# Performance work log

Measured on AMD Instinct MI355X. Metric: run time of the kernel, lower is better.

Reference implementation:

```python
import jax, jax.numpy as jnp
import numpy as np

D_MODEL = 1024
N_HEAD = 16
SEQ_LEN = 4096


def setup_inputs() -> dict:
    key = jax.random.key(0)
    ks = jax.random.split(key, 5)
    s = 0.02
    return {
        "x": jax.random.normal(ks[0], (SEQ_LEN, D_MODEL), dtype=jnp.float32),
        "w_qkv": jax.random.normal(ks[1], (D_MODEL, 3 * D_MODEL), dtype=jnp.float32) * s,
        "b_qkv": jnp.zeros((3 * D_MODEL,), dtype=jnp.float32),
        "w_o": jax.random.normal(ks[2], (D_MODEL, D_MODEL), dtype=jnp.float32) * s,
        "b_o": jnp.zeros((D_MODEL,), dtype=jnp.float32),
    }


def reference(x, w_qkv, b_qkv, w_o, b_o):
    seq_len, d_model = x.shape
    n_head = N_HEAD
    d_h = d_model // n_head

    qkv = x @ w_qkv + b_qkv                                  # [S, 3D]
    q, k, v = jnp.split(qkv, 3, axis=-1)                     # each [S, D]
    # [S, D] -> [H, S, d_h]
    q = q.reshape(seq_len, n_head, d_h).transpose(1, 0, 2)
    k = k.reshape(seq_len, n_head, d_h).transpose(1, 0, 2)
    v = v.reshape(seq_len, n_head, d_h).transpose(1, 0, 2)

    sim = jnp.einsum("hsd,htd->hst", q, k) / jnp.sqrt(jnp.float32(d_h))  # [H, S, S]
    causal = jnp.tril(jnp.ones((seq_len, seq_len), dtype=bool))[None]    # [1, S, S]
    neg_inf = jnp.finfo(sim.dtype).min
    sim = jnp.where(causal, sim, neg_inf)
    attn = jax.nn.softmax(sim, axis=-1)                                  # [H, S, S]
    out = jnp.einsum("hst,htd->hsd", attn, v)                            # [H, S, d_h]
    out = out.transpose(1, 0, 2).reshape(seq_len, d_model)               # [S, D]
    return out @ w_o + b_o
```

## Files before the change

kernel.cpp:

```cpp
#include <hip/hip_runtime.h>
#include <hip/hip_bf16.h>
#include <stdint.h>

typedef __bf16 bf16_t;
typedef __bf16 bf16x8 __attribute__((ext_vector_type(8)));
typedef float f32x4 __attribute__((ext_vector_type(4)));
typedef float f32x16 __attribute__((ext_vector_type(16)));

#define SEQ_LEN 4096
#define D_MODEL 1024
#define N_HEAD 16



__device__ __forceinline__ void gload_lds16(const void* g, void* lds) {
  __builtin_amdgcn_global_load_lds(
      (__attribute__((address_space(1))) void*)(g),
      (__attribute__((address_space(3))) void*)(lds), 16, 0, 0);
}

__device__ __forceinline__ unsigned short f2bfu(float f) {
  __bf16 h = (__bf16)f;
  return __builtin_bit_cast(unsigned short, h);
}

__device__ __forceinline__ unsigned cvt_pk_bf16(float a, float b) {
  unsigned r;
  asm("v_cvt_pk_bf16_f32 %0, %1, %2" : "=v"(r) : "v"(a), "v"(b));
  return r;
}


__global__ __launch_bounds__(256) void cvt_f32_bf16(const float* __restrict__ in,
                                                    bf16_t* __restrict__ out, int n) {
  int i = (blockIdx.x * 256 + threadIdx.x) * 4;
  if (i < n) {
    float4 v = *(const float4*)(in + i);
    unsigned int lo = (unsigned)f2bfu(v.x) | ((unsigned)f2bfu(v.y) << 16);
    unsigned int hi = (unsigned)f2bfu(v.z) | ((unsigned)f2bfu(v.w) << 16);
    uint2 pk; pk.x = lo; pk.y = hi;
    *(uint2*)(out + i) = pk;
  }
}

__global__ __launch_bounds__(256) void transpose_cvt(const float* __restrict__ W,
                                                     bf16_t* __restrict__ Wt,
                                                     int R, int C) {
  __shared__ float tile[64][65];
  const int tc = C >> 6;
  const int bc = blockIdx.x % tc;
  const int br = blockIdx.x / tc;
  #pragma unroll
  for (int p = 0; p < 16; ++p) {
    int idx = p * 256 + threadIdx.x;
    int i = idx >> 6, j = idx & 63;
    tile[i][j] = W[(size_t)(br * 64 + i) * C + bc * 64 + j];
  }
  __syncthreads();
  #pragma unroll
  for (int p = 0; p < 16; ++p) {
    int idx = p * 256 + threadIdx.x;
    int jj = idx >> 6, ii = idx & 63;
    Wt[(size_t)(bc * 64 + jj) * R + br * 64 + ii] = (bf16_t)tile[ii][jj];
  }
}


template <bool OUT_BF16, bool VSPLIT>
__global__ __launch_bounds__(256) void gemm_bt(const bf16_t* __restrict__ A,
                                               const bf16_t* __restrict__ Bt,
                                               const float* __restrict__ bias,
                                               void* __restrict__ Cout,
                                               bf16_t* __restrict__ qfout,
                                               bf16_t* __restrict__ kfout,
                                               bf16_t* __restrict__ vfout,
                                               int M, int N, int K) {
  __shared__ bf16_t As[128 * 32];
  __shared__ bf16_t Bs[128 * 32];
  const int tid = threadIdx.x;
  const int lane = tid & 63;
  const int w = tid >> 6;
  const int wr = (w >> 1) * 64;
  const int wc = (w & 1) * 64;
  const int i16 = lane & 15;
  const int g = lane >> 4;
  const int ntn = N >> 7;
  const int nwg = gridDim.x;
  const int bswz = (blockIdx.x & 7) * (nwg >> 3) + (blockIdx.x >> 3);
  const int bm = bswz / ntn;
  const int bn = bswz % ntn;
  const bf16_t* Abase = A + (size_t)(bm * 128) * K;
  const bf16_t* Bbase = Bt + (size_t)(bn * 128) * K;

  f32x4 acc[4][4];
  #pragma unroll
  for (int m = 0; m < 4; ++m)
    #pragma unroll
    for (int n = 0; n < 4; ++n)
      acc[m][n] = (f32x4){0.f, 0.f, 0.f, 0.f};

  for (int kt = 0; kt < K; kt += 32) {
    __syncthreads();
    #pragma unroll
    for (int p = 0; p < 2; ++p) {
      int idx = p * 256 + tid;
      int row = idx >> 2, ch = idx & 3;
      gload_lds16(Abase + (size_t)row * K + kt + ch * 8, (char*)As + idx * 16);
      gload_lds16(Bbase + (size_t)row * K + kt + ch * 8, (char*)Bs + idx * 16);
    }
    __syncthreads();
    bf16x8 af[4], bq[4];
    #pragma unroll
    for (int m = 0; m < 4; ++m)
      af[m] = *(const bf16x8*)(As + (wr + m * 16 + i16) * 32 + g * 8);
    #pragma unroll
    for (int n = 0; n < 4; ++n)
      bq[n] = *(const bf16x8*)(Bs + (wc + n * 16 + i16) * 32 + g * 8);
    #pragma unroll
    for (int m = 0; m < 4; ++m)
      #pragma unroll
      for (int n = 0; n < 4; ++n)
        acc[m][n] = __builtin_amdgcn_mfma_f32_16x16x32_bf16(af[m], bq[n], acc[m][n], 0, 0, 0);
  }

  #pragma unroll
  for (int m = 0; m < 4; ++m) {
    #pragma unroll
    for (int n = 0; n < 4; ++n) {
      int col = bn * 128 + wc + n * 16 + i16;
      float bv = bias ? bias[col] : 0.f;
      int row0 = bm * 128 + wr + m * 16 + g * 4;
      if (VSPLIT) {
        if (col < 2048) {
          const bool isK = (col >= 1024);
          const float scl = isK ? 0.18033688011112042f : 1.0f;
          bf16_t* base = isK ? kfout : qfout;
          int dg = col & 1023;
          int hh = dg >> 6, d = dg & 63;
          int ks = d >> 4, hib = (d >> 3) & 1, e = d & 7;
          int t = row0 >> 5, l0 = row0 & 31;
          bf16_t* fp = base + (size_t)hh * 262144 + t * 2048 + ks * 512 +
                       hib * 256 + l0 * 8 + e;
          #pragma unroll
          for (int r = 0; r < 4; ++r)
            fp[r * 8] = (bf16_t)((acc[m][n][r] + bv) * scl);
        } else {
          int dg = col - 2048;
          int hh = dg >> 6, dh = dg & 63;
          int dt = dh >> 5, l31v = dh & 31;
          int t = row0 >> 5, inner = row0 & 31;
          int g2 = inner >> 4, hiv = (inner >> 3) & 1, e0 = inner & 7;
          uint2 pk;
          pk.x = cvt_pk_bf16(acc[m][n][0] + bv, acc[m][n][1] + bv);
          pk.y = cvt_pk_bf16(acc[m][n][2] + bv, acc[m][n][3] + bv);
          *(uint2*)(vfout + (size_t)hh * 262144 + t * 2048 + dt * 1024 +
                    g2 * 512 + hiv * 256 + l31v * 8 + e0) = pk;
        }
      } else {
        #pragma unroll
        for (int r = 0; r < 4; ++r) {
          float v = acc[m][n][r] + bv;
          if (OUT_BF16)
            ((bf16_t*)Cout)[(size_t)(row0 + r) * N + col] = (bf16_t)v;
          else
            ((float*)Cout)[(size_t)(row0 + r) * N + col] = v;
        }
      }
    }
  }
}


__global__ __launch_bounds__(256) void attn_fwd(const bf16_t* __restrict__ qf_,
                                                const bf16_t* __restrict__ kf,
                                                const bf16_t* __restrict__ vf,
                                                bf16_t* __restrict__ aout) {
  __shared__ float Obuf[2][32][68];
  __shared__ float lpart[4][2][32];
  const int tid = threadIdx.x;
  const int w = tid >> 6;
  const int lane = tid & 63;
  const int l31 = lane & 31;
  const int hi = lane >> 5;
  const int bid = blockIdx.x;
  const int h = ((bid & 7) << 1) | ((bid >> 3) & 1);
  const int j = 127 - (bid >> 4);
  const int qg0 = j * 32;

  const bf16_t* qp = qf_ + (size_t)h * 262144 + (size_t)j * 2048 + hi * 256 + l31 * 8;
  bf16x8 qf[4];
  #pragma unroll
  for (int ks = 0; ks < 4; ++ks)
    qf[ks] = *(const bf16x8*)(qp + ks * 512);

  const bf16_t* kp = kf + (size_t)h * 262144 + hi * 256 + l31 * 8;
  const bf16_t* vp = vf + (size_t)h * 262144 + hi * 256 + l31 * 8;

  f32x16 ot0, ot1;
  #pragma unroll
  for (int r = 0; r < 16; ++r) { ot0[r] = 0.f; ot1[r] = 0.f; }
  float l_run = 0.f;

  const int nt = j + 1;
  bf16x8 kc[4], kn[4], vc[4];
  #pragma unroll
  for (int ks = 0; ks < 4; ++ks) {
    kc[ks] = *(const bf16x8*)(kp + w * 2048 + ks * 512);
    kn[ks] = kc[ks];
  }

  for (int t = w; t < nt; t += 4) {
    #pragma unroll
    for (int i = 0; i < 4; ++i) {
      int dt = i >> 1, g2 = i & 1;
      vc[i] = *(const bf16x8*)(vp + (size_t)t * 2048 + dt * 1024 + g2 * 512);
    }
    if (t + 4 < nt) {
      #pragma unroll
      for (int ks = 0; ks < 4; ++ks)
        kn[ks] = *(const bf16x8*)(kp + (size_t)(t + 4) * 2048 + ks * 512);
    }

    f32x16 s;
    #pragma unroll
    for (int r = 0; r < 16; ++r) s[r] = 0.f;
    __builtin_amdgcn_s_setprio(1);
    #pragma unroll
    for (int ks = 0; ks < 4; ++ks)
      s = __builtin_amdgcn_mfma_f32_32x32x16_bf16(kc[ks], qf[ks], s, 0, 0, 0);
    __builtin_amdgcn_s_setprio(0);

    if (t == nt - 1) {
      #pragma unroll
      for (int r = 0; r < 16; ++r) {
        int c = (r & 3) + 8 * (r >> 2) + 4 * hi;
        if (c > l31) s[r] = -1e30f;
      }
    }

    #pragma unroll
    for (int r = 0; r < 16; ++r)
      s[r] = __builtin_amdgcn_exp2f(s[r]);

    float sm[8];
    #pragma unroll
    for (int r = 0; r < 8; ++r) sm[r] = s[r] + s[r + 8];
    #pragma unroll
    for (int r = 0; r < 4; ++r) sm[r] = sm[r] + sm[r + 4];
    l_run += (sm[0] + sm[1]) + (sm[2] + sm[3]);

    bf16x8 pb[2];
    #pragma unroll
    for (int g2 = 0; g2 < 2; ++g2) {
      const int r0 = g2 * 8;
      unsigned a0 = cvt_pk_bf16(s[r0 + 0], s[r0 + 1]);
      unsigned a1 = cvt_pk_bf16(s[r0 + 2], s[r0 + 3]);
      unsigned b0 = cvt_pk_bf16(s[r0 + 4], s[r0 + 5]);
      unsigned b1 = cvt_pk_bf16(s[r0 + 6], s[r0 + 7]);
      unsigned X0 = hi ? a0 : b0;
      unsigned X1 = hi ? a1 : b1;
      unsigned Y0 = __shfl_xor(X0, 32);
      unsigned Y1 = __shfl_xor(X1, 32);
      uint4 f;
      f.x = hi ? Y0 : a0;
      f.y = hi ? Y1 : a1;
      f.z = hi ? b0 : Y0;
      f.w = hi ? b1 : Y1;
      pb[g2] = __builtin_bit_cast(bf16x8, f);
    }

    __builtin_amdgcn_s_setprio(1);
    ot0 = __builtin_amdgcn_mfma_f32_32x32x16_bf16(vc[0], pb[0], ot0, 0, 0, 0);
    ot0 = __builtin_amdgcn_mfma_f32_32x32x16_bf16(vc[1], pb[1], ot0, 0, 0, 0);
    ot1 = __builtin_amdgcn_mfma_f32_32x32x16_bf16(vc[2], pb[0], ot1, 0, 0, 0);
    ot1 = __builtin_amdgcn_mfma_f32_32x32x16_bf16(vc[3], pb[1], ot1, 0, 0, 0);
    __builtin_amdgcn_s_setprio(0);

    #pragma unroll
    for (int ks = 0; ks < 4; ++ks) kc[ks] = kn[ks];
  }

  lpart[w][hi][l31] = l_run;
  if (w >= 2) {
    #pragma unroll
    for (int dt = 0; dt < 2; ++dt) {
      const f32x16& o = dt ? ot1 : ot0;
      #pragma unroll
      for (int rq = 0; rq < 4; ++rq) {
        f32x4 qd;
        qd[0] = o[4 * rq + 0];
        qd[1] = o[4 * rq + 1];
        qd[2] = o[4 * rq + 2];
        qd[3] = o[4 * rq + 3];
        *(f32x4*)&Obuf[w - 2][l31][dt * 32 + 8 * rq + 4 * hi] = qd;
      }
    }
  }
  __syncthreads();
  if (w < 2) {
    #pragma unroll
    for (int dt = 0; dt < 2; ++dt) {
      const f32x16& o = dt ? ot1 : ot0;
      #pragma unroll
      for (int rq = 0; rq < 4; ++rq) {
        f32x4 qd = *(const f32x4*)&Obuf[w][l31][dt * 32 + 8 * rq + 4 * hi];
        qd[0] += o[4 * rq + 0];
        qd[1] += o[4 * rq + 1];
        qd[2] += o[4 * rq + 2];
        qd[3] += o[4 * rq + 3];
        *(f32x4*)&Obuf[w][l31][dt * 32 + 8 * rq + 4 * hi] = qd;
      }
    }
  }
  __syncthreads();
  #pragma unroll
  for (int iter = 0; iter < 8; ++iter) {
    int qq = w * 8 + iter;
    float sum = Obuf[0][qq][lane] + Obuf[1][qq][lane];
    float lst = lpart[0][0][qq] + lpart[0][1][qq] + lpart[1][0][qq] + lpart[1][1][qq] +
                lpart[2][0][qq] + lpart[2][1][qq] + lpart[3][0][qq] + lpart[3][1][qq];
    aout[(size_t)(qg0 + qq) * 1024 + h * 64 + lane] = (bf16_t)(sum / lst);
  }
}


extern "C" void kernel_launch(void* const* d_in, const int* in_sizes, int n_in,
                              void* d_out, int out_size, void* d_ws, size_t ws_size,
                              hipStream_t stream) {
  const float* x     = (const float*)d_in[0];
  const float* w_qkv = (const float*)d_in[1];
  const float* b_qkv = (const float*)d_in[2];
  const float* w_o   = (const float*)d_in[3];
  const float* b_o   = (const float*)d_in[4];

  char* ws = (char*)d_ws;
  bf16_t* xh    = (bf16_t*)(ws);
  bf16_t* wqkvT = (bf16_t*)(ws + 8388608);
  bf16_t* woT   = (bf16_t*)(ws + 14680064);
  bf16_t* qfb   = (bf16_t*)(ws + 16777216);
  bf16_t* kfb   = (bf16_t*)(ws + 25165824);
  bf16_t* vfb   = (bf16_t*)(ws + 33554432);
  bf16_t* aout  = (bf16_t*)(ws + 41943040);

  cvt_f32_bf16<<<(SEQ_LEN * D_MODEL) / 1024, 256, 0, stream>>>(x, xh, SEQ_LEN * D_MODEL);
  transpose_cvt<<<(1024 / 64) * (3072 / 64), 256, 0, stream>>>(w_qkv, wqkvT, 1024, 3072);
  transpose_cvt<<<(1024 / 64) * (1024 / 64), 256, 0, stream>>>(w_o, woT, 1024, 1024);

  gemm_bt<true, true><<<(4096 / 128) * (3072 / 128), 256, 0, stream>>>(
      xh, wqkvT, b_qkv, nullptr, qfb, kfb, vfb, 4096, 3072, 1024);

  attn_fwd<<<N_HEAD * (SEQ_LEN / 32), 256, 0, stream>>>(qfb, kfb, vfb, aout);

  gemm_bt<false, false><<<(4096 / 128) * (1024 / 128), 256, 0, stream>>>(
      aout, woT, b_o, d_out, nullptr, nullptr, nullptr, 4096, 1024, 1024);
}
```

Before: 141.0 us.

## Replace QKV projection GEMM with 256x256-tile, 8-wave pipelined LDS kernel

The QKV projection moves from the generic 128x128-tile gemm_bt to a dedicated kernel with 256x256 tiles, 512 threads, and a 128KB double-buffered LDS. Tiles are loaded directly into LDS, XOR-swizzled to avoid bank conflicts, and prefetched across phases using explicit vmcnt waits, barriers and setprio around the MFMA bursts. The aim is more data reuse per tile and overlap of global loads with matrix math in the largest GEMM. The cost is only 192 workgroups for 256 CUs, which can leave compute units idle, plus more complex hand-scheduled synchronisation. The old templated gemm_bt is reduced to the float-output path used by the output projection.

```diff
diff --git a/kernel.cpp b/kernel.cpp
--- a/kernel.cpp
+++ b/kernel.cpp
@@ -29,6 +29,8 @@
   asm("v_cvt_pk_bf16_f32 %0, %1, %2" : "=v"(r) : "v"(a), "v"(b));
   return r;
 }
+
+#define CBAR() asm volatile("" ::: "memory")
 
 
 __global__ __launch_bounds__(256) void cvt_f32_bf16(const float* __restrict__ in,
@@ -66,14 +68,160 @@
 }
 
 
-template <bool OUT_BF16, bool VSPLIT>
+__device__ __forceinline__ void stage_half(const bf16_t* src, char* ldsbase,
+                                           int w, int srow, int schunk) {
+  const bf16_t* s0 = src + (size_t)(w * 8 + srow) * 1024 + schunk * 8;
+  char* d0 = ldsbase + w * 1024;
+  gload_lds16(s0, d0);
+  gload_lds16(s0 + 64 * 1024, d0 + 8192);
+}
+
+__global__ __launch_bounds__(512, 2) void gemm1_8p(const bf16_t* __restrict__ A,
+                                                   const bf16_t* __restrict__ Bt,
+                                                   const float* __restrict__ bias,
+                                                   bf16_t* __restrict__ qfout,
+                                                   bf16_t* __restrict__ kfout,
+                                                   bf16_t* __restrict__ vfout) {
+  __shared__ char ldsbuf[131072];
+  const int tid = threadIdx.x;
+  const int lane = tid & 63;
+  const int w = tid >> 6;
+  const int wm = w >> 2;
+  const int wn = w & 3;
+  const int i16 = lane & 15;
+  const int g = lane >> 4;
+  const int hi = lane >> 5;
+  const int bswz = (blockIdx.x & 7) * 24 + (blockIdx.x >> 3);
+  const int bm = bswz / 12;
+  const int bn = bswz % 12;
+
+  const int srow = lane >> 3;
+  const int schunk = (lane & 7) ^ (hi << 1);
+  const int s5 = ((i16 >> 2) & 1) << 5;
+
+  auto stA = [&](int buf, int half, int kt) {
+    stage_half(A + (size_t)(bm * 256 + half * 128) * 1024 + kt * 64,
+               ldsbuf + buf * 32768 + half * 16384, w, srow, schunk);
+  };
+  auto stB = [&](int buf, int half, int kt) {
+    stage_half(Bt + (size_t)(bn * 256 + half * 128) * 1024 + kt * 64,
+               ldsbuf + 65536 + buf * 32768 + half * 16384, w, srow, schunk);
+  };
+
+  f32x4 acc[8][4];
+  #pragma unroll
+  for (int m = 0; m < 8; ++m)
+    #pragma unroll
+    for (int n = 0; n < 4; ++n)
+      acc[m][n] = (f32x4){0.f, 0.f, 0.f, 0.f};
+
+  const int browbase = (wn & 1) * 64;
+
+  stA(0, 0, 0); stA(0, 1, 0); stB(0, 0, 0); stB(0, 1, 0);
+  stB(1, 0, 1); stB(1, 1, 1);
+  asm volatile("s_waitcnt vmcnt(4)" ::: "memory");
+  CBAR(); __builtin_amdgcn_s_barrier(); CBAR();
+
+  bf16x8 bfr[4][2];
+
+  for (int i = 0; i < 8; ++i) {
+    const int t1 = 2 * i + 1, t2 = 2 * i + 2, t3 = 2 * i + 3;
+    #pragma unroll
+    for (int p = 0; p < 8; ++p) {
+      const int buf = p >> 2;
+      const int q = p & 3;
+      const char* aB = ldsbuf + buf * 32768 + wm * 16384;
+      const char* bB = ldsbuf + 65536 + buf * 32768 + (wn >> 1) * 16384;
+      if (q == 0) {
+        #pragma unroll
+        for (int n = 0; n < 4; ++n)
+          #pragma unroll
+          for (int ks = 0; ks < 2; ++ks) {
+            int U = (browbase + n * 16 + i16) * 128 + ks * 64 + g * 16;
+            bfr[n][ks] = *(const bf16x8*)(bB + (U ^ s5));
+          }
+      }
+      bf16x8 af[2][2];
+      #pragma unroll
+      for (int mm = 0; mm < 2; ++mm)
+        #pragma unroll
+        for (int ks = 0; ks < 2; ++ks) {
+          int U = ((q * 2 + mm) * 16 + i16) * 128 + ks * 64 + g * 16;
+          af[mm][ks] = *(const bf16x8*)(aB + (U ^ s5));
+        }
+      if (p == 0)      stA(1, 0, t1);
+      else if (p == 1) stA(1, 1, t1);
+      else if (p == 2) { if (t2 < 16) stB(0, 0, t2); }
+      else if (p == 3) { if (t2 < 16) stB(0, 1, t2); }
+      else if (p == 4) { if (t2 < 16) stA(0, 0, t2); }
+      else if (p == 5) { if (t2 < 16) stA(0, 1, t2); }
+      else if (p == 6) { if (t3 < 16) stB(1, 0, t3); }
+      else             { if (t3 < 16) stB(1, 1, t3); }
+
+      CBAR(); __builtin_amdgcn_s_barrier(); CBAR();
+
+      __builtin_amdgcn_s_setprio(1);
+      #pragma unroll
+      for (int mm = 0; mm < 2; ++mm)
+        #pragma unroll
+        for (int n = 0; n < 4; ++n)
+          #pragma unroll
+          for (int ks = 0; ks < 2; ++ks)
+            acc[q * 2 + mm][n] = __builtin_amdgcn_mfma_f32_16x16x32_bf16(
+                af[mm][ks], bfr[n][ks], acc[q * 2 + mm][n], 0, 0, 0);
+      __builtin_amdgcn_s_setprio(0);
+
+      if (p == 3) {
+        if (i == 7) asm volatile("s_waitcnt vmcnt(0)" ::: "memory");
+        else        asm volatile("s_waitcnt vmcnt(4)" ::: "memory");
+      } else if (p == 7 && i < 7) {
+        asm volatile("s_waitcnt vmcnt(4)" ::: "memory");
+      }
+      CBAR(); __builtin_amdgcn_s_barrier(); CBAR();
+    }
+  }
+
+  #pragma unroll
+  for (int m = 0; m < 8; ++m) {
+    #pragma unroll
+    for (int n = 0; n < 4; ++n) {
+      int col = bn * 256 + wn * 64 + n * 16 + i16;
+      float bv = bias[col];
+      int row0 = bm * 256 + wm * 128 + m * 16 + g * 4;
+      if (col < 2048) {
+        const bool isK = (col >= 1024);
+        const float scl = isK ? 0.18033688011112042f : 1.0f;
+        bf16_t* base = isK ? kfout : qfout;
+        int dg = col & 1023;
+        int hh = dg >> 6, d = dg & 63;
+        int ks = d >> 4, hib = (d >> 3) & 1, e = d & 7;
+        int t = row0 >> 5, l0 = row0 & 31;
+        bf16_t* fp = base + (size_t)hh * 262144 + t * 2048 + ks * 512 +
+                     hib * 256 + l0 * 8 + e;
+        #pragma unroll
+        for (int r = 0; r < 4; ++r)
+          fp[r * 8] = (bf16_t)((acc[m][n][r] + bv) * scl);
+      } else {
+        int dg = col - 2048;
+        int hh = dg >> 6, dh = dg & 63;
+        int dt = dh >> 5, l31v = dh & 31;
+        int t = row0 >> 5, inner = row0 & 31;
+        int g2 = inner >> 4, hiv = (inner >> 3) & 1, e0 = inner & 7;
+        uint2 pk;
+        pk.x = cvt_pk_bf16(acc[m][n][0] + bv, acc[m][n][1] + bv);
+        pk.y = cvt_pk_bf16(acc[m][n][2] + bv, acc[m][n][3] + bv);
+        *(uint2*)(vfout + (size_t)hh * 262144 + t * 2048 + dt * 1024 +
+                  g2 * 512 + hiv * 256 + l31v * 8 + e0) = pk;
+      }
+    }
+  }
+}
+
+
 __global__ __launch_bounds__(256) void gemm_bt(const bf16_t* __restrict__ A,
                                                const bf16_t* __restrict__ Bt,
                                                const float* __restrict__ bias,
-                                               void* __restrict__ Cout,
-                                               bf16_t* __restrict__ qfout,
-                                               bf16_t* __restrict__ kfout,
-                                               bf16_t* __restrict__ vfout,
+                                               float* __restrict__ Cout,
                                                int M, int N, int K) {
   __shared__ bf16_t As[128 * 32];
   __shared__ bf16_t Bs[128 * 32];
@@ -130,42 +278,9 @@
       int col = bn * 128 + wc + n * 16 + i16;
       float bv = bias ? bias[col] : 0.f;
       int row0 = bm * 128 + wr + m * 16 + g * 4;
-      if (VSPLIT) {
-        if (col < 2048) {
-          const bool isK = (col >= 1024);
-          const float scl = isK ? 0.18033688011112042f : 1.0f;
-          bf16_t* base = isK ? kfout : qfout;
-          int dg = col & 1023;
-          int hh = dg >> 6, d = dg & 63;
-          int ks = d >> 4, hib = (d >> 3) & 1, e = d & 7;
-          int t = row0 >> 5, l0 = row0 & 31;
-          bf16_t* fp = base + (size_t)hh * 262144 + t * 2048 + ks * 512 +
-                       hib * 256 + l0 * 8 + e;
-          #pragma unroll
-          for (int r = 0; r < 4; ++r)
-            fp[r * 8] = (bf16_t)((acc[m][n][r] + bv) * scl);
-        } else {
-          int dg = col - 2048;
-          int hh = dg >> 6, dh = dg & 63;
-          int dt = dh >> 5, l31v = dh & 31;
-          int t = row0 >> 5, inner = row0 & 31;
-          int g2 = inner >> 4, hiv = (inner >> 3) & 1, e0 = inner & 7;
-          uint2 pk;
-          pk.x = cvt_pk_bf16(acc[m][n][0] + bv, acc[m][n][1] + bv);
-          pk.y = cvt_pk_bf16(acc[m][n][2] + bv, acc[m][n][3] + bv);
-          *(uint2*)(vfout + (size_t)hh * 262144 + t * 2048 + dt * 1024 +
-                    g2 * 512 + hiv * 256 + l31v * 8 + e0) = pk;
-        }
-      } else {
-        #pragma unroll
-        for (int r = 0; r < 4; ++r) {
-          float v = acc[m][n][r] + bv;
-          if (OUT_BF16)
-            ((bf16_t*)Cout)[(size_t)(row0 + r) * N + col] = (bf16_t)v;
-          else
-            ((float*)Cout)[(size_t)(row0 + r) * N + col] = v;
-        }
-      }
+      #pragma unroll
+      for (int r = 0; r < 4; ++r)
+        Cout[(size_t)(row0 + r) * N + col] = acc[m][n][r] + bv;
     }
   }
 }
@@ -346,11 +461,10 @@
   transpose_cvt<<<(1024 / 64) * (3072 / 64), 256, 0, stream>>>(w_qkv, wqkvT, 1024, 3072);
   transpose_cvt<<<(1024 / 64) * (1024 / 64), 256, 0, stream>>>(w_o, woT, 1024, 1024);
 
-  gemm_bt<true, true><<<(4096 / 128) * (3072 / 128), 256, 0, stream>>>(
-      xh, wqkvT, b_qkv, nullptr, qfb, kfb, vfb, 4096, 3072, 1024);
+  gemm1_8p<<<192, 512, 0, stream>>>(xh, wqkvT, b_qkv, qfb, kfb, vfb);
 
   attn_fwd<<<N_HEAD * (SEQ_LEN / 32), 256, 0, stream>>>(qfb, kfb, vfb, aout);
 
-  gemm_bt<false, false><<<(4096 / 128) * (1024 / 128), 256, 0, stream>>>(
-      aout, woT, b_o, d_out, nullptr, nullptr, nullptr, 4096, 1024, 1024);
-}
+  gemm_bt<<<(4096 / 128) * (1024 / 128), 256, 0, stream>>>(
+      aout, woT, b_o, (float*)d_out, 4096, 1024, 1024);
+}
```

Result: faster. 136.2 us (-3.4%).
